# Performance work log

Measured on AMD Instinct MI355X. Metric: run time of the kernel, lower is better.

The kernel has to match this reference:

```python
import jax, jax.numpy as jnp
import numpy as np

B, C, H, W = 16, 64, 64, 64
K_CLUST, KS, OUT, RANK, MLP = 16, 3, 64, 8, 32
F = C * KS * KS  # 576


def setup_inputs() -> dict:
    key = jax.random.key(0)
    ks = jax.random.split(key, 14)
    rn = lambda k, shp, s=0.05: (jax.random.normal(k, shp, jnp.float32) * s)
    return {
        "x": jax.random.normal(ks[0], (B, C, H, W), jnp.float32),
        "labels": jax.random.randint(ks[1], (B, H, W), 0, K_CLUST),
        "lr_w1": rn(ks[2], (F, MLP)), "lr_b1": rn(ks[3], (MLP,)),
        "lr_w2": rn(ks[4], (MLP, MLP)), "lr_b2": rn(ks[5], (MLP,)),
        "lr_w3": rn(ks[6], (MLP, RANK)), "lr_b3": rn(ks[7], (RANK,)),
        "base_kernels": rn(ks[8], (RANK, F, OUT), 0.1),
        "bw1": rn(ks[9], (F, MLP)), "bb1": rn(ks[10], (MLP,)),
        "bw2": rn(ks[11], (MLP, OUT)), "bb2": rn(ks[12], (OUT,)),
    }


def _extract_patches(x):
    # torch nn.Unfold(kernel=3, padding=1) layout: features ordered (C, kh, kw)
    b, c, h, w = x.shape
    xp = jnp.pad(x, ((0, 0), (0, 0), (1, 1), (1, 1)))
    p = jnp.stack([xp[:, :, i:i + h, j:j + w] for i in range(KS) for j in range(KS)], axis=2)  # [B,C,9,H,W]
    return p.reshape(b, c * KS * KS, h * w).transpose(0, 2, 1)  # [B, HW, F]


def reference(x, labels, lr_w1, lr_b1, lr_w2, lr_b2, lr_w3, lr_b3,
              base_kernels, bw1, bb1, bw2, bb2):
    b, c, h, w = x.shape
    patches = _extract_patches(x)                              # [B, HW, F]
    lab = labels.reshape(b, -1)                                # [B, HW]
    onehot = jax.nn.one_hot(lab, K_CLUST, dtype=patches.dtype) # [B, HW, K]
    counts = onehot.sum(axis=1)                                # [B, K]
    centers = jnp.einsum('bnk,bnf->bkf', onehot, patches) / (counts[:, :, None] + 1e-6)

    hdn = jax.nn.relu(centers @ lr_w1 + lr_b1)
    hdn = jax.nn.relu(hdn @ lr_w2 + lr_b2)
    lowrank = hdn @ lr_w3 + lr_b3                              # [B, K, R]
    bias = jax.nn.relu(centers @ bw1 + bb1) @ bw2 + bb2        # [B, K, O]

    kernels = jnp.einsum('bkr,rfo->bkfo', lowrank, base_kernels)   # [B, K, F, O]
    scores = jnp.einsum('bnf,bkfo->bnko', patches, kernels)        # [B, HW, K, O]
    out = jnp.einsum('bnko,bnk->bno', scores, onehot)
    out = out + jnp.einsum('bko,bnk->bno', bias, onehot)           # per-pixel cluster bias
    return out.reshape(b, h, w, OUT).transpose(0, 3, 1, 2)         # [B, O, H, W]
```

## Files before the change

### kernel.cpp

```cpp
#include <hip/hip_runtime.h>
#include <stdint.h>
#include <stddef.h>

#define NB   16
#define NC   64
#define NH   64
#define NW   64
#define KC   16
#define NOUT 64
#define NRANK 8
#define NMLP 32
#define NF   576
#define NPIX 4096
#define XH   66

typedef short s16x8 __attribute__((ext_vector_type(8)));
typedef short s16x4 __attribute__((ext_vector_type(4)));
typedef float f32x4 __attribute__((ext_vector_type(4)));

__device__ __forceinline__ unsigned short f2bf(float x) {
    union { float f; uint32_t u; } v; v.f = x;
    uint32_t r = v.u + 0x7FFFu + ((v.u >> 16) & 1u);
    return (unsigned short)(r >> 16);
}
__device__ __forceinline__ float bf2f(unsigned short u) {
    union { uint32_t u; float f; } v; v.u = ((uint32_t)u) << 16;
    return v.f;
}

extern "C" __global__ __launch_bounds__(256)
void k_prep_all(const float* __restrict__ x, const float* __restrict__ basek,
                unsigned short* __restrict__ xcl, unsigned short* __restrict__ basekF)
{
    __shared__ float tile[64 * 65];
    const int blk0 = blockIdx.x;
    const int tid = threadIdx.x;
    if (blk0 < XH * 16) {
        const int b = blk0 & 15, yy = blk0 >> 4;
        unsigned short* dst = xcl + ((size_t)(b * XH + yy) * XH) * 64;
        if (yy == 0 || yy == XH - 1) {
            for (int e = tid; e < XH * 64; e += 256) dst[e] = 0;
            return;
        }
        const int y = yy - 1;
        const float* src = x + (size_t)b * NC * (NH * NW) + y * NW;
        #pragma unroll
        for (int rr = 0; rr < 16; ++rr) {
            int c = rr * 4 + (tid >> 6);
            int xx = tid & 63;
            tile[c * 65 + xx] = src[(size_t)c * (NH * NW) + xx];
        }
        __syncthreads();
        for (int ee = tid; ee < 528; ee += 256) {
            int xx = ee >> 3;
            int c0 = (ee & 7) * 8;
            s16x8 v;
            #pragma unroll
            for (int j = 0; j < 8; ++j) {
                float f = (xx == 0 || xx == XH - 1) ? 0.f : tile[(c0 + j) * 65 + (xx - 1)];
                v[j] = (short)f2bf(f);
            }
            *reinterpret_cast<s16x8*>(dst + ee * 8) = v;
        }
    } else {
        const int blk = blk0 - XH * 16;
        const int ks = blk >> 2, wv = blk & 3;
        unsigned short outv[16];
        #pragma unroll
        for (int i = 0; i < 16; ++i) {
            int e = tid * 16 + i;
            int r = e >> 9;
            int lane = (e >> 3) & 63;
            int j = e & 7;
            int col = wv * 16 + (lane & 15);
            int fp = (lane >> 4) * 8 + ks * 32 + j;
            int tap = fp >> 6, c = fp & 63;
            outv[i] = f2bf(basek[((size_t)r * NF + c * 9 + tap) * NOUT + col]);
        }
        unsigned short* dst = basekF + (size_t)blk * 4096 + tid * 16;
        #pragma unroll
        for (int i = 0; i < 16; ++i) dst[i] = outv[i];
    }
}

extern "C" __global__ __launch_bounds__(576)
void k_centers(const unsigned short* __restrict__ xcl, const int* __restrict__ labels,
               const float* __restrict__ lw1, const float* __restrict__ lb1,
               const float* __restrict__ lw2, const float* __restrict__ lb2,
               const float* __restrict__ lw3, const float* __restrict__ lb3,
               const float* __restrict__ bw1, const float* __restrict__ bb1,
               const float* __restrict__ bw2, const float* __restrict__ bb2,
               const unsigned short* __restrict__ basekF,
               unsigned short* __restrict__ lists, unsigned short* __restrict__ slotmap,
               int* __restrict__ counts, float* __restrict__ biasrows,
               unsigned short* __restrict__ wt)
{
    const int bk = blockIdx.x;
    const int b = bk & 15, k = bk >> 4;
    __shared__ unsigned short list[NPIX];
    __shared__ int cntr;
    __shared__ float cbuf[NF];
    __shared__ float p1[8][NMLP], pb[8][NMLP];
    __shared__ float h1[NMLP], h2[NMLP], hb[NMLP], lrs[NRANK];
    const int tid = threadIdx.x;
    const int lane = tid & 63, wv = tid >> 6;
    const int* lab = labels + b * NPIX;

    if (tid == 0) cntr = 0;
    __syncthreads();

    for (int base = 0; base < NPIX; base += 576) {
        int n = base + tid;
        bool pred = (n < NPIX) && (lab[n] == k);
        unsigned long long m = __ballot(pred);
        int pre = __popcll(m & ((1ull << lane) - 1ull));
        int wb = 0;
        if (lane == 0) wb = atomicAdd(&cntr, __popcll(m));
        wb = __shfl(wb, 0);
        if (pred) {
            int slot = wb + pre;
            list[slot] = (unsigned short)n;
            slotmap[b * NPIX + n] = (unsigned short)slot;
        }
    }
    __syncthreads();
    const int cnt = cntr;
    unsigned short* gl = lists + bk * NPIX;
    for (int i = tid; i < cnt; i += 576) gl[i] = list[i];
    if (tid == 0) counts[bk] = cnt;

    const int tap = wv;
    const int pg = lane >> 4, cq = lane & 15;
    const int dy = tap / 3, dx = tap - dy * 3;
    const unsigned short* xb = xcl + (size_t)b * (XH * XH * 64);
    float s0 = 0.f, s1 = 0.f, s2 = 0.f, s3 = 0.f;
    #pragma unroll 2
    for (int i = pg; i < cnt; i += 4) {
        int n = list[i];
        const unsigned short* pr = xb + ((((n >> 6) + dy) * XH) + (n & 63) + dx) * 64 + cq * 4;
        s16x4 vv = *reinterpret_cast<const s16x4*>(pr);
        s0 += bf2f((unsigned short)vv[0]);
        s1 += bf2f((unsigned short)vv[1]);
        s2 += bf2f((unsigned short)vv[2]);
        s3 += bf2f((unsigned short)vv[3]);
    }
    s0 += __shfl_xor(s0, 16); s0 += __shfl_xor(s0, 32);
    s1 += __shfl_xor(s1, 16); s1 += __shfl_xor(s1, 32);
    s2 += __shfl_xor(s2, 16); s2 += __shfl_xor(s2, 32);
    s3 += __shfl_xor(s3, 16); s3 += __shfl_xor(s3, 32);
    const float inv = 1.f / ((float)cnt + 1e-6f);
    if (pg == 0) {
        cbuf[(cq * 4 + 0) * 9 + tap] = s0 * inv;
        cbuf[(cq * 4 + 1) * 9 + tap] = s1 * inv;
        cbuf[(cq * 4 + 2) * 9 + tap] = s2 * inv;
        cbuf[(cq * 4 + 3) * 9 + tap] = s3 * inv;
    }
    __syncthreads();

    if (tid < 256) {
        const int j = tid & 31, ch = tid >> 5;
        float a1 = 0.f, a2 = 0.f;
        for (int i = 0; i < 72; ++i) {
            int f = ch * 72 + i;
            float cv = cbuf[f];
            a1 += cv * lw1[f * NMLP + j];
            a2 += cv * bw1[f * NMLP + j];
        }
        p1[ch][j] = a1; pb[ch][j] = a2;
    }
    __syncthreads();
    if (tid < NMLP) {
        float a = lb1[tid];
        for (int i = 0; i < 8; ++i) a += p1[i][tid];
        h1[tid] = fmaxf(a, 0.f);
    } else if (tid < 2 * NMLP) {
        int j = tid - NMLP;
        float a = bb1[j];
        for (int i = 0; i < 8; ++i) a += pb[i][j];
        hb[j] = fmaxf(a, 0.f);
    }
    __syncthreads();
    if (tid < NMLP) {
        float a = lb2[tid];
        for (int i = 0; i < NMLP; ++i) a += h1[i] * lw2[i * NMLP + tid];
        h2[tid] = fmaxf(a, 0.f);
    } else if (tid >= 64 && tid < 128) {
        int o = tid - 64;
        float a = bb2[o];
        for (int i = 0; i < NMLP; ++i) a += hb[i] * bw2[i * NOUT + o];
        biasrows[bk * NOUT + o] = a;
    }
    __syncthreads();
    if (tid < NRANK) {
        float a = lb3[tid];
        for (int i = 0; i < NMLP; ++i) a += h2[i] * lw3[i * NRANK + tid];
        lrs[tid] = a;
    }
    __syncthreads();

    float l8[NRANK];
    #pragma unroll
    for (int r = 0; r < NRANK; ++r) l8[r] = lrs[r];
    unsigned short* wtg = wt + (size_t)bk * (18 * 2048);
    #pragma unroll 1
    for (int q = 0; q < 8; ++q) {
        int m = q * 576 + tid;
        int ks = m >> 8, t = m & 255;
        const unsigned short* src = basekF
            + ((size_t)(ks * 4 + (t >> 6)) * 8) * 512 + (t & 63) * 8;
        float w[8] = {0.f, 0.f, 0.f, 0.f, 0.f, 0.f, 0.f, 0.f};
        #pragma unroll
        for (int r = 0; r < NRANK; ++r) {
            s16x8 bv = *reinterpret_cast<const s16x8*>(src + r * 512);
            #pragma unroll
            for (int j = 0; j < 8; ++j)
                w[j] += l8[r] * bf2f((unsigned short)bv[j]);
        }
        s16x8 f;
        #pragma unroll
        for (int j = 0; j < 8; ++j) f[j] = (short)f2bf(w[j]);
        *reinterpret_cast<s16x8*>(wtg + ks * 2048 + t * 8) = f;
    }
}

extern "C" __global__ __launch_bounds__(256)
void k_main(const unsigned short* __restrict__ xcl, const unsigned short* __restrict__ lists,
            const int* __restrict__ counts, const unsigned short* __restrict__ wt,
            const float* __restrict__ biasrows, unsigned short* __restrict__ outc)
{
    const int blk = blockIdx.x;
    const int bk = blk & 255, split = blk >> 8;
    const int b = bk & 15, k = bk >> 4;
    const int tid = threadIdx.x;
    const int lane = tid & 63, wv = tid >> 6;
    const int quad = lane >> 4, l16 = lane & 15;
    const int cnt = counts[bk];
    int prefix = 0;
    for (int kk = 0; kk < k; ++kk) prefix += counts[kk * 16 + b];

    __shared__ __align__(16) unsigned short albuf[32 * 584];
    __shared__ float biasl[NOUT];

    if (tid < NOUT) biasl[tid] = biasrows[bk * NOUT + tid];

    const int col = wv * 16 + l16;
    const unsigned short* wsrc = wt + (size_t)bk * (18 * 2048) + tid * 8;
    s16x8 bfr[18];
    #pragma unroll
    for (int ks = 0; ks < 18; ++ks)
        bfr[ks] = *reinterpret_cast<const s16x8*>(wsrc + ks * 2048);

    const unsigned short* xb = xcl + (size_t)b * (XH * XH * 64);
    const unsigned short* gl = lists + bk * NPIX;
    const int p = tid >> 3, part = tid & 7;
    const int ntile = (cnt + 31) >> 5;

    for (int t = split; t < ntile; t += 4) {
        int slot = (t << 5) + p;
        int n = (slot < cnt) ? (int)gl[slot] : 0;
        const unsigned short* xrow = xb + (((n >> 6) * XH) + (n & 63)) * 64 + part * 8;
        unsigned short* arow = albuf + p * 584 + part * 8;
        #pragma unroll
        for (int tap = 0; tap < 9; ++tap) {
            int dy = tap / 3, dx = tap - dy * 3;
            *reinterpret_cast<s16x8*>(arow + tap * 64) =
                *reinterpret_cast<const s16x8*>(xrow + (dy * XH + dx) * 64);
        }
        __syncthreads();

        f32x4 acc0 = {0.f, 0.f, 0.f, 0.f}, acc1 = {0.f, 0.f, 0.f, 0.f};
        const unsigned short* ar0 = albuf + l16 * 584 + quad * 8;
        const unsigned short* ar1 = ar0 + 16 * 584;
        #pragma unroll
        for (int ks = 0; ks < 18; ++ks) {
            s16x8 a0 = *reinterpret_cast<const s16x8*>(ar0 + ks * 32);
            s16x8 a1 = *reinterpret_cast<const s16x8*>(ar1 + ks * 32);
            acc0 = __builtin_amdgcn_mfma_f32_16x16x32_bf16(a0, bfr[ks], acc0, 0, 0, 0);
            acc1 = __builtin_amdgcn_mfma_f32_16x16x32_bf16(a1, bfr[ks], acc1, 0, 0, 0);
        }
        __syncthreads();

        float bb = biasl[col];
        unsigned short* ob = outc + ((size_t)b * NPIX + prefix) * 64;
        #pragma unroll
        for (int r = 0; r < 4; ++r) {
            int s0 = (t << 5) + quad * 4 + r;
            if (s0 < cnt) ob[(size_t)s0 * 64 + col] = f2bf(acc0[r] + bb);
            int s1 = s0 + 16;
            if (s1 < cnt) ob[(size_t)s1 * 64 + col] = f2bf(acc1[r] + bb);
        }
    }
}

extern "C" __global__ __launch_bounds__(256)
void k_scatter(const int* __restrict__ labels, const unsigned short* __restrict__ slotmap,
               const int* __restrict__ counts, const unsigned short* __restrict__ outc,
               float* __restrict__ out)
{
    const int blk = blockIdx.x;
    const int b = blk & 15, chunk = blk >> 4;
    const int tid = threadIdx.x;
    __shared__ int pref[KC];
    __shared__ int sptr[256];
    __shared__ unsigned short tile[256 * 68];
    if (tid < KC) {
        int s = 0;
        for (int kk = 0; kk < tid; ++kk) s += counts[kk * 16 + b];
        pref[tid] = s;
    }
    __syncthreads();
    const int n0 = chunk * 256;
    {
        int n = n0 + tid;
        int kk = labels[b * NPIX + n];
        sptr[tid] = pref[kk] + (int)slotmap[b * NPIX + n];
    }
    __syncthreads();
    const int pixb = tid >> 3, part = tid & 7;
    #pragma unroll
    for (int pass = 0; pass < 8; ++pass) {
        int pix = pass * 32 + pixb;
        int ptr = sptr[pix];
        s16x8 vv = *reinterpret_cast<const s16x8*>(
            outc + ((size_t)b * NPIX + ptr) * 64 + part * 8);
        s16x4 lo = {vv[0], vv[1], vv[2], vv[3]};
        s16x4 hi = {vv[4], vv[5], vv[6], vv[7]};
        *reinterpret_cast<s16x4*>(&tile[pix * 68 + part * 8]) = lo;
        *reinterpret_cast<s16x4*>(&tile[pix * 68 + part * 8 + 4]) = hi;
    }
    __syncthreads();
    float* ob = out + (size_t)b * NOUT * NPIX + n0 + tid;
    #pragma unroll
    for (int o2 = 0; o2 < 32; ++o2) {
        uint32_t pair = *reinterpret_cast<const uint32_t*>(&tile[tid * 68 + o2 * 2]);
        ob[(size_t)(2 * o2) * NPIX]     = bf2f((unsigned short)(pair & 0xffffu));
        ob[(size_t)(2 * o2 + 1) * NPIX] = bf2f((unsigned short)(pair >> 16));
    }
}

extern "C" void kernel_launch(void* const* d_in, const int* in_sizes, int n_in,
                              void* d_out, int out_size, void* d_ws, size_t ws_size,
                              hipStream_t stream)
{
    const float* x      = (const float*)d_in[0];
    const int*   labels = (const int*)d_in[1];
    const float* lw1    = (const float*)d_in[2];
    const float* lb1    = (const float*)d_in[3];
    const float* lw2    = (const float*)d_in[4];
    const float* lb2    = (const float*)d_in[5];
    const float* lw3    = (const float*)d_in[6];
    const float* lb3    = (const float*)d_in[7];
    const float* basek  = (const float*)d_in[8];
    const float* bw1    = (const float*)d_in[9];
    const float* bb1    = (const float*)d_in[10];
    const float* bw2    = (const float*)d_in[11];
    const float* bb2    = (const float*)d_in[12];
    float* out = (float*)d_out;

    char* ws = (char*)d_ws;
    unsigned short* lists   = (unsigned short*)(ws);
    int*            counts  = (int*)(ws + 2097152);
    float*          biasrows= (float*)(ws + 2098176);
    unsigned short* basekF  = (unsigned short*)(ws + 2163712);
    unsigned short* slotmap = (unsigned short*)(ws + 2753536);
    unsigned short* xcl     = (unsigned short*)(ws + 2884608);
    unsigned short* outc    = (unsigned short*)(ws + 11805696);
    unsigned short* wt      = (unsigned short*)(ws + 20194304);

    k_prep_all<<<XH * 16 + 72, 256, 0, stream>>>(x, basek, xcl, basekF);
    k_centers<<<256, 576, 0, stream>>>(xcl, labels, lw1, lb1, lw2, lb2, lw3, lb3,
                                       bw1, bb1, bw2, bb2, basekF,
                                       lists, slotmap, counts, biasrows, wt);
    k_main<<<1024, 256, 0, stream>>>(xcl, lists, counts, wt, biasrows, outc);
    k_scatter<<<256, 256, 0, stream>>>(labels, slotmap, counts, outc, out);
}
```

Before: 147.1 us.

## Widen centers kernel to 1024 threads with ordered compaction and split scatter

k_centers now runs with 1024 threads. The atomic-based list compaction becomes a deterministic per-wave prefix scan. Each wave now gathers all 9 taps for one pixel per iteration, with a cross-wave reduction in shared memory, instead of one wave per tap. k_scatter is split four ways over output channels, so 1024 blocks each handle 16 channels with a smaller LDS tile, which should improve occupancy and parallelism. The scalar bf16 loads in the gather and the extra syncs per compaction chunk may offset the gains.

```diff
diff --git a/kernel.cpp b/kernel.cpp
--- a/kernel.cpp
+++ b/kernel.cpp
@@ -83,7 +83,7 @@
     }
 }
 
-extern "C" __global__ __launch_bounds__(576)
+extern "C" __global__ __launch_bounds__(1024)
 void k_centers(const unsigned short* __restrict__ xcl, const int* __restrict__ labels,
                const float* __restrict__ lw1, const float* __restrict__ lb1,
                const float* __restrict__ lw2, const float* __restrict__ lb2,
@@ -98,7 +98,8 @@
     const int bk = blockIdx.x;
     const int b = bk & 15, k = bk >> 4;
     __shared__ unsigned short list[NPIX];
-    __shared__ int cntr;
+    __shared__ int wcnt[16];
+    __shared__ float wsum[16 * 9 * 64];
     __shared__ float cbuf[NF];
     __shared__ float p1[8][NMLP], pb[8][NMLP];
     __shared__ float h1[NMLP], h2[NMLP], hb[NMLP], lrs[NRANK];
@@ -106,54 +107,67 @@
     const int lane = tid & 63, wv = tid >> 6;
     const int* lab = labels + b * NPIX;
 
-    if (tid == 0) cntr = 0;
-    __syncthreads();
-
-    for (int base = 0; base < NPIX; base += 576) {
+    int total = 0;
+    #pragma unroll 1
+    for (int base = 0; base < NPIX; base += 1024) {
         int n = base + tid;
-        bool pred = (n < NPIX) && (lab[n] == k);
+        bool pred = (lab[n] == k);
         unsigned long long m = __ballot(pred);
+        if (lane == 0) wcnt[wv] = __popcll(m);
         int pre = __popcll(m & ((1ull << lane) - 1ull));
-        int wb = 0;
-        if (lane == 0) wb = atomicAdd(&cntr, __popcll(m));
-        wb = __shfl(wb, 0);
+        __syncthreads();
+        int wbase = total;
+        for (int i = 0; i < wv; ++i) wbase += wcnt[i];
+        int nt = total;
+        for (int i = 0; i < 16; ++i) nt += wcnt[i];
         if (pred) {
-            int slot = wb + pre;
+            int slot = wbase + pre;
             list[slot] = (unsigned short)n;
             slotmap[b * NPIX + n] = (unsigned short)slot;
         }
-    }
-    __syncthreads();
-    const int cnt = cntr;
-    unsigned short* gl = lists + bk * NPIX;
-    for (int i = tid; i < cnt; i += 576) gl[i] = list[i];
+        total = nt;
+        __syncthreads();
+    }
+    const int cnt = total;
+    for (int i = tid; i < cnt; i += 1024) lists[bk * NPIX + i] = list[i];
     if (tid == 0) counts[bk] = cnt;
-
-    const int tap = wv;
-    const int pg = lane >> 4, cq = lane & 15;
-    const int dy = tap / 3, dx = tap - dy * 3;
-    const unsigned short* xb = xcl + (size_t)b * (XH * XH * 64);
-    float s0 = 0.f, s1 = 0.f, s2 = 0.f, s3 = 0.f;
-    #pragma unroll 2
-    for (int i = pg; i < cnt; i += 4) {
+    __syncthreads();
+
+    float s00 = 0.f, s01 = 0.f, s02 = 0.f,
+          s10 = 0.f, s11 = 0.f, s12 = 0.f,
+          s20 = 0.f, s21 = 0.f, s22 = 0.f;
+    const unsigned short* xb = xcl + (size_t)b * (XH * XH * 64) + lane;
+    #pragma unroll 1
+    for (int i = wv; i < cnt; i += 16) {
         int n = list[i];
-        const unsigned short* pr = xb + ((((n >> 6) + dy) * XH) + (n & 63) + dx) * 64 + cq * 4;
-        s16x4 vv = *reinterpret_cast<const s16x4*>(pr);
-        s0 += bf2f((unsigned short)vv[0]);
-        s1 += bf2f((unsigned short)vv[1]);
-        s2 += bf2f((unsigned short)vv[2]);
-        s3 += bf2f((unsigned short)vv[3]);
-    }
-    s0 += __shfl_xor(s0, 16); s0 += __shfl_xor(s0, 32);
-    s1 += __shfl_xor(s1, 16); s1 += __shfl_xor(s1, 32);
-    s2 += __shfl_xor(s2, 16); s2 += __shfl_xor(s2, 32);
-    s3 += __shfl_xor(s3, 16); s3 += __shfl_xor(s3, 32);
+        const unsigned short* p0 = xb + (((n >> 6) * XH) + (n & 63)) * 64;
+        s00 += bf2f(p0[0]);
+        s01 += bf2f(p0[64]);
+        s02 += bf2f(p0[128]);
+        const unsigned short* prow1 = p0 + XH * 64;
+        s10 += bf2f(prow1[0]);
+        s11 += bf2f(prow1[64]);
+        s12 += bf2f(prow1[128]);
+        const unsigned short* prow2 = p0 + 2 * XH * 64;
+        s20 += bf2f(prow2[0]);
+        s21 += bf2f(prow2[64]);
+        s22 += bf2f(prow2[128]);
+    }
+    {
+        float* wrow = wsum + wv * 576 + lane;
+        wrow[0 * 64] = s00; wrow[1 * 64] = s01; wrow[2 * 64] = s02;
+        wrow[3 * 64] = s10; wrow[4 * 64] = s11; wrow[5 * 64] = s12;
+        wrow[6 * 64] = s20; wrow[7 * 64] = s21; wrow[8 * 64] = s22;
+    }
+    __syncthreads();
+
     const float inv = 1.f / ((float)cnt + 1e-6f);
-    if (pg == 0) {
-        cbuf[(cq * 4 + 0) * 9 + tap] = s0 * inv;
-        cbuf[(cq * 4 + 1) * 9 + tap] = s1 * inv;
-        cbuf[(cq * 4 + 2) * 9 + tap] = s2 * inv;
-        cbuf[(cq * 4 + 3) * 9 + tap] = s3 * inv;
+    if (tid < NF) {
+        int tap = tid >> 6, c = tid & 63;
+        float s = 0.f;
+        #pragma unroll
+        for (int w = 0; w < 16; ++w) s += wsum[w * 576 + tap * 64 + c];
+        cbuf[c * 9 + tap] = s * inv;
     }
     __syncthreads();
 
@@ -203,23 +217,25 @@
     for (int r = 0; r < NRANK; ++r) l8[r] = lrs[r];
     unsigned short* wtg = wt + (size_t)bk * (18 * 2048);
     #pragma unroll 1
-    for (int q = 0; q < 8; ++q) {
-        int m = q * 576 + tid;
-        int ks = m >> 8, t = m & 255;
-        const unsigned short* src = basekF
-            + ((size_t)(ks * 4 + (t >> 6)) * 8) * 512 + (t & 63) * 8;
-        float w[8] = {0.f, 0.f, 0.f, 0.f, 0.f, 0.f, 0.f, 0.f};
-        #pragma unroll
-        for (int r = 0; r < NRANK; ++r) {
-            s16x8 bv = *reinterpret_cast<const s16x8*>(src + r * 512);
+    for (int q = 0; q < 5; ++q) {
+        int m = q * 1024 + tid;
+        if (m < 4608) {
+            int ks = m >> 8, t = m & 255;
+            const unsigned short* src = basekF
+                + ((size_t)(ks * 4 + (t >> 6)) * 8) * 512 + (t & 63) * 8;
+            float w[8] = {0.f, 0.f, 0.f, 0.f, 0.f, 0.f, 0.f, 0.f};
             #pragma unroll
-            for (int j = 0; j < 8; ++j)
-                w[j] += l8[r] * bf2f((unsigned short)bv[j]);
-        }
-        s16x8 f;
-        #pragma unroll
-        for (int j = 0; j < 8; ++j) f[j] = (short)f2bf(w[j]);
-        *reinterpret_cast<s16x8*>(wtg + ks * 2048 + t * 8) = f;
+            for (int r = 0; r < NRANK; ++r) {
+                s16x8 bv = *reinterpret_cast<const s16x8*>(src + r * 512);
+                #pragma unroll
+                for (int j = 0; j < 8; ++j)
+                    w[j] += l8[r] * bf2f((unsigned short)bv[j]);
+            }
+            s16x8 f;
+            #pragma unroll
+            for (int j = 0; j < 8; ++j) f[j] = (short)f2bf(w[j]);
+            *reinterpret_cast<s16x8*>(wtg + ks * 2048 + t * 8) = f;
+        }
     }
 }
 
@@ -298,11 +314,11 @@
                float* __restrict__ out)
 {
     const int blk = blockIdx.x;
-    const int b = blk & 15, chunk = blk >> 4;
+    const int b = blk & 15, chunk = (blk >> 4) & 15, q = blk >> 8;
     const int tid = threadIdx.x;
     __shared__ int pref[KC];
     __shared__ int sptr[256];
-    __shared__ unsigned short tile[256 * 68];
+    __shared__ unsigned short tt[256 * 20];
     if (tid < KC) {
         int s = 0;
         for (int kk = 0; kk < tid; ++kk) s += counts[kk * 16 + b];
@@ -312,30 +328,25 @@
     const int n0 = chunk * 256;
     {
         int n = n0 + tid;
-        int kk = labels[b * NPIX + n];
-        sptr[tid] = pref[kk] + (int)slotmap[b * NPIX + n];
-    }
-    __syncthreads();
-    const int pixb = tid >> 3, part = tid & 7;
+        sptr[tid] = pref[labels[b * NPIX + n]] + (int)slotmap[b * NPIX + n];
+    }
+    __syncthreads();
     #pragma unroll
-    for (int pass = 0; pass < 8; ++pass) {
-        int pix = pass * 32 + pixb;
-        int ptr = sptr[pix];
+    for (int e0 = 0; e0 < 2; ++e0) {
+        int e = e0 * 256 + tid;
+        int pix = e >> 1, part = e & 1;
         s16x8 vv = *reinterpret_cast<const s16x8*>(
-            outc + ((size_t)b * NPIX + ptr) * 64 + part * 8);
+            outc + ((size_t)b * NPIX + sptr[pix]) * 64 + q * 16 + part * 8);
         s16x4 lo = {vv[0], vv[1], vv[2], vv[3]};
         s16x4 hi = {vv[4], vv[5], vv[6], vv[7]};
-        *reinterpret_cast<s16x4*>(&tile[pix * 68 + part * 8]) = lo;
-        *reinterpret_cast<s16x4*>(&tile[pix * 68 + part * 8 + 4]) = hi;
-    }
-    __syncthreads();
-    float* ob = out + (size_t)b * NOUT * NPIX + n0 + tid;
+        *reinterpret_cast<s16x4*>(tt + pix * 20 + part * 8) = lo;
+        *reinterpret_cast<s16x4*>(tt + pix * 20 + part * 8 + 4) = hi;
+    }
+    __syncthreads();
+    float* ob = out + ((size_t)(b * NOUT + q * 16)) * NPIX + n0;
     #pragma unroll
-    for (int o2 = 0; o2 < 32; ++o2) {
-        uint32_t pair = *reinterpret_cast<const uint32_t*>(&tile[tid * 68 + o2 * 2]);
-        ob[(size_t)(2 * o2) * NPIX]     = bf2f((unsigned short)(pair & 0xffffu));
-        ob[(size_t)(2 * o2 + 1) * NPIX] = bf2f((unsigned short)(pair >> 16));
-    }
+    for (int oo = 0; oo < 16; ++oo)
+        ob[(size_t)oo * NPIX + tid] = bf2f(tt[tid * 20 + oo]);
 }
 
 extern "C" void kernel_launch(void* const* d_in, const int* in_sizes, int n_in,
@@ -368,9 +379,9 @@
     unsigned short* wt      = (unsigned short*)(ws + 20194304);
 
     k_prep_all<<<XH * 16 + 72, 256, 0, stream>>>(x, basek, xcl, basekF);
-    k_centers<<<256, 576, 0, stream>>>(xcl, labels, lw1, lb1, lw2, lb2, lw3, lb3,
-                                       bw1, bb1, bw2, bb2, basekF,
-                                       lists, slotmap, counts, biasrows, wt);
+    k_centers<<<256, 1024, 0, stream>>>(xcl, labels, lw1, lb1, lw2, lb2, lw3, lb3,
+                                        bw1, bb1, bw2, bb2, basekF,
+                                        lists, slotmap, counts, biasrows, wt);
     k_main<<<1024, 256, 0, stream>>>(xcl, lists, counts, wt, biasrows, outc);
-    k_scatter<<<256, 256, 0, stream>>>(labels, slotmap, counts, outc, out);
-}
+    k_scatter<<<1024, 256, 0, stream>>>(labels, slotmap, counts, outc, out);
+}
```

After: 139.5 us. -5.2%, faster.
